# Performance work log

Hardware: AMD Instinct MI355X
Metric: run time of the kernel (lower is better)

The kernel has to match this reference:

```python
import jax, jax.numpy as jnp
import numpy as np

EMBED, HEADS, LEVELS, POINTS, FFN = 256, 8, 4, 4, 1024
HD = EMBED // HEADS


def layer_norm(x, g, b, eps=1e-5):
    m = jnp.mean(x, axis=-1, keepdims=True)
    v = jnp.mean((x - m) ** 2, axis=-1, keepdims=True)
    return (x - m) / jnp.sqrt(v + eps) * g + b


def ms_deform_attn_core(value, shapes_np, loc, attn):
    # value: (B, nk, H, hd); loc: (B, nq, H, L, P, 2) normalized [0,1]; attn: (B, nq, H, L, P)
    B, nq = loc.shape[0], loc.shape[1]
    splits = np.cumsum(shapes_np[:, 0] * shapes_np[:, 1])[:-1]
    vals = jnp.split(value, splits, axis=1)
    out = jnp.zeros((B, HEADS, nq, HD), value.dtype)
    for l in range(LEVELS):
        Hl, Wl = int(shapes_np[l, 0]), int(shapes_np[l, 1])
        v = vals[l].transpose(0, 2, 1, 3)                     # (B, H, Hl*Wl, hd)
        x = loc[:, :, :, l, :, 0] * Wl - 0.5                  # (B, nq, H, P) pixel coords
        y = loc[:, :, :, l, :, 1] * Hl - 0.5
        x0 = jnp.floor(x); y0 = jnp.floor(y)
        fx = x - x0; fy = y - y0
        x0i = x0.astype(jnp.int32); y0i = y0.astype(jnp.int32)
        acc = jnp.zeros((B, HEADS, nq * POINTS, HD), value.dtype)
        for dx, dy, w in ((0, 0, (1 - fx) * (1 - fy)), (1, 0, fx * (1 - fy)),
                          (0, 1, (1 - fx) * fy), (1, 1, fx * fy)):
            xi = x0i + dx; yi = y0i + dy
            valid = (xi >= 0) & (xi < Wl) & (yi >= 0) & (yi < Hl)
            idx = jnp.clip(yi, 0, Hl - 1) * Wl + jnp.clip(xi, 0, Wl - 1)  # (B, nq, H, P)
            idx_f = idx.transpose(0, 2, 1, 3).reshape(B, HEADS, -1)
            g = jnp.take_along_axis(v, idx_f[..., None], axis=2)          # (B, H, nq*P, hd)
            wv = jnp.where(valid, w, 0.0).transpose(0, 2, 1, 3).reshape(B, HEADS, -1, 1)
            acc = acc + g * wv
        aw = attn[:, :, :, l].transpose(0, 2, 1, 3).reshape(B, HEADS, -1, 1)
        out = out + (acc * aw).reshape(B, HEADS, nq, POINTS, HD).sum(3)
    return out.transpose(0, 2, 1, 3).reshape(B, nq, EMBED)


def setup_inputs() -> dict:
    key = jax.random.key(0)
    ks = jax.random.split(key, 20)
    B = 2
    shapes = np.array([[136, 136], [68, 68], [34, 34], [17, 17]], np.int32)
    nk = int((shapes[:, 0] * shapes[:, 1]).sum())  # 24565
    lsi = np.concatenate([[0], np.cumsum(shapes[:, 0] * shapes[:, 1])[:-1]]).astype(np.int32)

    def lin(k, i, o):
        return jax.random.normal(k, (i, o), jnp.float32) * 0.02

    return {
        "src": jax.random.normal(ks[0], (B, nk, EMBED), jnp.float32),
        "reference_points": jax.random.uniform(ks[1], (B, nk, LEVELS, 2), jnp.float32),
        "spatial_shapes": jnp.asarray(shapes),
        "level_start_index": jnp.asarray(lsi),
        "w_off": lin(ks[2], EMBED, HEADS * LEVELS * POINTS * 2),
        "b_off": jax.random.normal(ks[3], (HEADS * LEVELS * POINTS * 2,), jnp.float32) * 0.5,
        "w_att": lin(ks[4], EMBED, HEADS * LEVELS * POINTS),
        "b_att": jnp.zeros((HEADS * LEVELS * POINTS,), jnp.float32),
        "w_val": lin(ks[5], EMBED, EMBED), "b_val": jnp.zeros((EMBED,), jnp.float32),
        "w_out": lin(ks[6], EMBED, EMBED), "b_out": jnp.zeros((EMBED,), jnp.float32),
        "g1": jnp.ones((EMBED,), jnp.float32), "bt1": jnp.zeros((EMBED,), jnp.float32),
        "w1": lin(ks[7], EMBED, FFN), "b1": jnp.zeros((FFN,), jnp.float32),
        "w2": lin(ks[8], FFN, EMBED), "b2": jnp.zeros((EMBED,), jnp.float32),
        "g2": jnp.ones((EMBED,), jnp.float32), "bt2": jnp.zeros((EMBED,), jnp.float32),
    }


def reference(src, reference_points, spatial_shapes, level_start_index,
              w_off, b_off, w_att, b_att, w_val, b_val, w_out, b_out,
              g1, bt1, w1, b1, w2, b2, g2, bt2):
    B, nq, D = src.shape
    shapes_np = np.asarray(spatial_shapes)
    # projections
    value = (src @ w_val + b_val).reshape(B, nq, HEADS, HD)
    off = (src @ w_off + b_off).reshape(B, nq, HEADS, LEVELS, POINTS, 2)
    attn = (src @ w_att + b_att).reshape(B, nq, HEADS, LEVELS * POINTS)
    attn = jax.nn.softmax(attn, axis=-1).reshape(B, nq, HEADS, LEVELS, POINTS)
    # sampling locations: ref + offset / [W, H] per level
    normalizer = jnp.asarray(shapes_np[:, ::-1].copy(), src.dtype)  # (L, 2) = [W, H]
    loc = reference_points[:, :, None, :, None, :] + off / normalizer[None, None, None, :, None, :]
    attn_out = ms_deform_attn_core(value, shapes_np, loc, attn) @ w_out + b_out
    x = layer_norm(src + attn_out, g1, bt1)
    ffn = jax.nn.relu(x @ w1 + b1) @ w2 + b2
    return layer_norm(x + ffn, g2, bt2)
```

## Files before the change

### kernel.cpp

```cpp
#include <hip/hip_runtime.h>
#include <math.h>

#define EMBED 256
#define HEADS 8
#define LEVELS 4
#define POINTS 4
#define FFNDIM 1024

typedef float f32x4 __attribute__((ext_vector_type(4)));
typedef float f32x2 __attribute__((ext_vector_type(2)));
typedef __bf16 bf16x8 __attribute__((ext_vector_type(8)));

static __device__ __forceinline__ float4 ld4f(const float* p) {
    return *reinterpret_cast<const float4*>(p);
}
static __device__ __forceinline__ unsigned short f2bf(float f) {
    unsigned int u = __float_as_uint(f);
    unsigned int r = (u + 0x7fffu + ((u >> 16) & 1u)) >> 16;
    return (unsigned short)r;
}
static __device__ __forceinline__ float bf2f(unsigned short u) {
    return __uint_as_float((unsigned int)u << 16);
}
static __device__ __forceinline__ f32x2 pkfma(f32x2 a, f32x2 b, f32x2 c) {
#if __has_builtin(__builtin_elementwise_fma)
    return __builtin_elementwise_fma(a, b, c);
#else
    f32x2 r; r.x = fmaf(a.x, b.x, c.x); r.y = fmaf(a.y, b.y, c.y); return r;
#endif
}
static __device__ __forceinline__
void gl_lds16(const unsigned short* g, unsigned short* l) {
    __builtin_amdgcn_global_load_lds(
        (const __attribute__((address_space(1))) unsigned int*)g,
        (__attribute__((address_space(3))) unsigned int*)l, 16, 0, 0);
}

__global__ __launch_bounds__(256)
void k_cvt_src(const float* __restrict__ src, unsigned short* __restrict__ dst, int n)
{
    int i = (blockIdx.x * 256 + threadIdx.x) * 4;
    const int stride = gridDim.x * 1024;
    for (; i < n; i += stride) {
        float4 v = ld4f(src + i);
        ushort4 o;
        o.x = f2bf(v.x); o.y = f2bf(v.y); o.z = f2bf(v.z); o.w = f2bf(v.w);
        *reinterpret_cast<ushort4*>(dst + i) = o;
    }
}

__global__ __launch_bounds__(256)
void k_cvt_w(const float* __restrict__ wv, const float* __restrict__ wo,
             const float* __restrict__ wa, const float* __restrict__ wout,
             const float* __restrict__ w1, const float* __restrict__ w2,
             unsigned short* __restrict__ wcat, unsigned short* __restrict__ woutt,
             unsigned short* __restrict__ w1t, unsigned short* __restrict__ w2t)
{
    const int total = 163840 + 65536 + 262144 + 262144;
    for (int gid = blockIdx.x * 256 + threadIdx.x; gid < total; gid += gridDim.x * 256) {
        int local = gid;
        float f; unsigned short* dst;
        if (local < 163840) {
            int n = local >> 8, k = local & 255;
            if (n < 256)      f = wv[k * 256 + n];
            else if (n < 512) f = wo[k * 256 + (n - 256)];
            else              f = wa[k * 128 + (n - 512)];
            dst = wcat + local;
        } else if ((local -= 163840) < 65536) {
            int n = local >> 8, k = local & 255;
            f = wout[k * 256 + n];
            dst = woutt + local;
        } else if ((local -= 65536) < 262144) {
            int n = local >> 8, k = local & 255;
            f = w1[k * 1024 + n];
            dst = w1t + local;
        } else {
            local -= 262144;
            int n = local >> 10, k = local & 1023;
            f = w2[k * 256 + n];
            dst = w2t + local;
        }
        *dst = f2bf(f);
    }
}


#define GEMM_STAGE(Aptr, ASTR, Wptr, WSTR, kcexp)                              \
    {                                                                          \
        int row = (wid << 3) + (lane >> 3);                                    \
        int slot = (lane & 7) ^ (row & 7);                                     \
        gl_lds16(Aptr + (size_t)(m0 + row) * ASTR + (kcexp) * 64 + slot * 8,   \
                 a_s + (size_t)(wid << 3) * 64);                               \
    }                                                                          \
    _Pragma("unroll")                                                          \
    for (int rnd = 0; rnd < 4; ++rnd) {                                        \
        int row = (rnd << 6) + (wid << 3) + (lane >> 3);                       \
        int slot = (lane & 7) ^ (row & 7);                                     \
        gl_lds16(Wptr + (size_t)(n0 + row) * WSTR + (kcexp) * 64 + slot * 8,   \
                 w_s + (size_t)((rnd << 6) + (wid << 3)) * 64);                \
    }

#define GEMM_FRAGS_MFMA                                                        \
    {                                                                          \
        bf16x8 af[2][2], bfr[4][2];                                            \
        const int ksb = (lane >> 4);                                           \
        _Pragma("unroll")                                                      \
        for (int i = 0; i < 2; ++i) {                                          \
            int m = wm * 32 + i * 16 + cl;                                     \
            _Pragma("unroll")                                                  \
            for (int kk = 0; kk < 2; ++kk) {                                   \
                int phys = (kk * 4 + ksb) ^ (m & 7);                           \
                af[i][kk] = *reinterpret_cast<const bf16x8*>(                  \
                    a_s + m * 64 + phys * 8);                                  \
            }                                                                  \
        }                                                                      \
        _Pragma("unroll")                                                      \
        for (int j = 0; j < 4; ++j) {                                          \
            int n = wn * 64 + j * 16 + cl;                                     \
            _Pragma("unroll")                                                  \
            for (int kk = 0; kk < 2; ++kk) {                                   \
                int phys = (kk * 4 + ksb) ^ (n & 7);                           \
                bfr[j][kk] = *reinterpret_cast<const bf16x8*>(                 \
                    w_s + n * 64 + phys * 8);                                  \
            }                                                                  \
        }                                                                      \
        _Pragma("unroll")                                                      \
        for (int kk = 0; kk < 2; ++kk)                                         \
            _Pragma("unroll")                                                  \
            for (int i = 0; i < 2; ++i)                                        \
                _Pragma("unroll")                                              \
                for (int j = 0; j < 4; ++j)                                    \
                    acc[i][j] = __builtin_amdgcn_mfma_f32_16x16x32_bf16(       \
                        af[i][kk], bfr[j][kk], acc[i][j], 0, 0, 0);            \
    }

__global__ __launch_bounds__(512)
void k_proj(const unsigned short* __restrict__ A, const unsigned short* __restrict__ Wt,
            const float* __restrict__ b_val, const float* __restrict__ b_off,
            const float* __restrict__ b_att,
            unsigned short* __restrict__ value, unsigned short* __restrict__ offr,
            unsigned short* __restrict__ attw, int M, int nk)
{
    __shared__ __align__(16) unsigned short smem[20480];
    unsigned short* a_s = smem;
    unsigned short* w_s = smem + 4096;
    const int tid = threadIdx.x;
    const int m0 = blockIdx.x * 64;
    const int y = blockIdx.y;
    const int n0 = y * 256;
    const int lane = tid & 63, wid = tid >> 6;
    const int wm = wid >> 2, wn = wid & 3;
    const int cl = lane & 15, r4 = (lane >> 4) * 4;

    f32x4 acc[2][4] = {};

    for (int kc = 0; kc < 4; ++kc) {
        __syncthreads();
        GEMM_STAGE(A, 256, Wt, 256, kc)
        __syncthreads();
        GEMM_FRAGS_MFMA
    }

    if (y < 2) {
        const float* bias = (y == 0) ? b_val : b_off;
        __syncthreads();
        #pragma unroll
        for (int j = 0; j < 4; ++j) {
            int col = wn * 64 + j * 16 + cl;
            float bv = bias[col];
            #pragma unroll
            for (int i = 0; i < 2; ++i)
                #pragma unroll
                for (int r = 0; r < 4; ++r)
                    smem[(wm * 32 + i * 16 + r4 + r) * 264 + col] = f2bf(acc[i][j][r] + bv);
        }
        __syncthreads();
        if (y == 0) {
            #pragma unroll
            for (int t = 0; t < 4; ++t) {
                int idx = tid + t * 512;
                int row = idx >> 5, cu = idx & 31;
                int grow = m0 + row;
                if (grow < M) {
                    int b = grow >= nk;
                    int pix = grow - (b ? nk : 0);
                    int hh = cu >> 2, ch = (cu & 3) * 8;
                    *reinterpret_cast<uint4*>(
                        value + ((size_t)(b * 8 + hh) * nk + pix) * 32 + ch) =
                        *reinterpret_cast<const uint4*>(smem + row * 264 + cu * 8);
                }
            }
        } else {
            #pragma unroll
            for (int t = 0; t < 4; ++t) {
                int idx = tid + t * 512;
                int row = idx >> 5, cu = idx & 31;
                int grow = m0 + row;
                if (grow < M)
                    *reinterpret_cast<uint4*>(offr + (size_t)grow * 256 + cu * 8) =
                        *reinterpret_cast<const uint4*>(smem + row * 264 + cu * 8);
            }
        }
    } else {
        if (wn < 2) {
            #pragma unroll
            for (int j = 0; j < 4; ++j) {
                int a = wn * 64 + j * 16 + cl;
                float bv = b_att[a];
                #pragma unroll
                for (int i = 0; i < 2; ++i) {
                    #pragma unroll
                    for (int r = 0; r < 4; ++r) {
                        float v = acc[i][j][r] + bv;
                        float mx = v;
                        mx = fmaxf(mx, __shfl_xor(mx, 1));
                        mx = fmaxf(mx, __shfl_xor(mx, 2));
                        mx = fmaxf(mx, __shfl_xor(mx, 4));
                        mx = fmaxf(mx, __shfl_xor(mx, 8));
                        float e = __expf(v - mx);
                        float s = e;
                        s += __shfl_xor(s, 1);
                        s += __shfl_xor(s, 2);
                        s += __shfl_xor(s, 4);
                        s += __shfl_xor(s, 8);
                        acc[i][j][r] = e / s;
                    }
                }
            }
        }
        __syncthreads();
        if (wn < 2) {
            #pragma unroll
            for (int j = 0; j < 4; ++j) {
                int a = wn * 64 + j * 16 + cl;
                #pragma unroll
                for (int i = 0; i < 2; ++i)
                    #pragma unroll
                    for (int r = 0; r < 4; ++r)
                        smem[(wm * 32 + i * 16 + r4 + r) * 136 + a] = f2bf(acc[i][j][r]);
            }
        }
        __syncthreads();
        #pragma unroll
        for (int t = 0; t < 2; ++t) {
            int idx = tid + t * 512;
            int row = idx >> 4, cu = idx & 15;
            int grow = m0 + row;
            if (grow < M)
                *reinterpret_cast<uint4*>(attw + (size_t)grow * 128 + cu * 8) =
                    *reinterpret_cast<const uint4*>(smem + row * 136 + cu * 8);
        }
    }
}

__global__ __launch_bounds__(256)
void k_sample(const unsigned short* __restrict__ value,
              const unsigned short* __restrict__ offr,
              const unsigned short* __restrict__ attw,
              const float* __restrict__ ref,
              const int* __restrict__ shapes, const int* __restrict__ lsi,
              unsigned short* __restrict__ core, int M)
{
    __shared__ int2 iw_s[8][8][65];
    const int tid = threadIdx.x;
    const int tok0 = blockIdx.x * 8;
    const int nk = lsi[3] + shapes[6] * shapes[7];

    #pragma unroll
    for (int q = 0; q < 4; ++q) {
        const int task = tid + q * 256;
        const int tl = task >> 7;
        const int rest = task & 127;
        const int l = (rest >> 2) & 3;
        const int lp = rest & 15;
        const int hh = rest >> 4;
        const int tok = tok0 + tl;
        int2 out[4];
        if (tok < M) {
            const int Hl = shapes[l * 2], Wl = shapes[l * 2 + 1];
            const int bh = ((tok >= nk) ? 8 : 0) + hh;
            const int pbase = bh * nk + lsi[l];
            const float rx = ref[(size_t)tok * 8 + l * 2];
            const float ry = ref[(size_t)tok * 8 + l * 2 + 1];
            const unsigned int oxy =
                *reinterpret_cast<const unsigned int*>(offr + (size_t)tok * 256 + rest * 2);
            const float ox = bf2f((unsigned short)(oxy & 0xffffu));
            const float oy = bf2f((unsigned short)(oxy >> 16));
            const float aw = bf2f(attw[(size_t)tok * 128 + rest]);
            const float x = fmaf(rx, (float)Wl, ox) - 0.5f;
            const float y = fmaf(ry, (float)Hl, oy) - 0.5f;
            const float x0f = floorf(x), y0f = floorf(y);
            const float fx = x - x0f, fy = y - y0f;
            const int x0 = (int)x0f, y0 = (int)y0f;
            #pragma unroll
            for (int t = 0; t < 4; ++t) {
                const int dx = t & 1, dy = t >> 1;
                const int xi = x0 + dx, yi = y0 + dy;
                const bool valid = (xi >= 0) & (xi < Wl) & (yi >= 0) & (yi < Hl);
                const float w = (dx ? fx : 1.f - fx) * (dy ? fy : 1.f - fy) * aw;
                const int xc = min(max(xi, 0), Wl - 1);
                const int yc = min(max(yi, 0), Hl - 1);
                out[t].x = (pbase + yc * Wl + xc) * 16;
                out[t].y = __float_as_int(valid ? w : 0.f);
            }
        } else {
            #pragma unroll
            for (int t = 0; t < 4; ++t) out[t] = make_int2(0, 0);
        }
        #pragma unroll
        for (int t = 0; t < 4; ++t)
            iw_s[tl][hh][lp * 4 + t] = out[t];
    }
    __syncthreads();

    const int tl = tid >> 5;
    const int h = (tid >> 2) & 7;
    const int dp = tid & 3;
    const int tok = tok0 + tl;
    const unsigned int* vu = reinterpret_cast<const unsigned int*>(value) + dp * 4;
    const int2* pt = &iw_s[tl][h][0];
    f32x2 a0 = {0.f, 0.f}, a1 = {0.f, 0.f};
    f32x2 a2 = {0.f, 0.f}, a3 = {0.f, 0.f};
    #pragma unroll 16
    for (int q = 0; q < 64; ++q) {
        const int2 iw = pt[q];
        const float w = __int_as_float(iw.y);
        const f32x2 w2 = {w, w};
        const uint4 v = *reinterpret_cast<const uint4*>(vu + (size_t)(unsigned)iw.x);
        const f32x2 v0 = {__uint_as_float(v.x << 16), __uint_as_float(v.x & 0xffff0000u)};
        const f32x2 v1 = {__uint_as_float(v.y << 16), __uint_as_float(v.y & 0xffff0000u)};
        const f32x2 v2 = {__uint_as_float(v.z << 16), __uint_as_float(v.z & 0xffff0000u)};
        const f32x2 v3 = {__uint_as_float(v.w << 16), __uint_as_float(v.w & 0xffff0000u)};
        a0 = pkfma(v0, w2, a0);
        a1 = pkfma(v1, w2, a1);
        a2 = pkfma(v2, w2, a2);
        a3 = pkfma(v3, w2, a3);
    }
    if (tok < M) {
        uint4 o;
        o.x = (unsigned int)f2bf(a0.x) | ((unsigned int)f2bf(a0.y) << 16);
        o.y = (unsigned int)f2bf(a1.x) | ((unsigned int)f2bf(a1.y) << 16);
        o.z = (unsigned int)f2bf(a2.x) | ((unsigned int)f2bf(a2.y) << 16);
        o.w = (unsigned int)f2bf(a3.x) | ((unsigned int)f2bf(a3.y) << 16);
        *reinterpret_cast<uint4*>(core + (size_t)tok * 256 + h * 32 + dp * 8) = o;
    }
}

__global__ __launch_bounds__(512)
void k_oproj(const unsigned short* __restrict__ A, const unsigned short* __restrict__ Wt,
             const float* __restrict__ b_out, const float* __restrict__ src,
             const float* __restrict__ g1, const float* __restrict__ bt1,
             unsigned short* __restrict__ X, int M)
{
    __shared__ __align__(16) unsigned short smem[20480];
    unsigned short* a_s = smem;
    unsigned short* w_s = smem + 4096;
    __shared__ float red[64 * 8];
    __shared__ float mr[64 * 2];
    const int tid = threadIdx.x;
    const int m0 = blockIdx.x * 64;
    const int n0 = 0;
    const int lane = tid & 63, wid = tid >> 6;
    const int wm = wid >> 2, wn = wid & 3;
    const int cl = lane & 15, r4 = (lane >> 4) * 4;

    f32x4 acc[2][4] = {};

    for (int kc = 0; kc < 4; ++kc) {
        __syncthreads();
        GEMM_STAGE(A, 256, Wt, 256, kc)
        __syncthreads();
        GEMM_FRAGS_MFMA
    }

    #pragma unroll
    for (int j = 0; j < 4; ++j) {
        int col = wn * 64 + j * 16 + cl;
        float bv = b_out[col];
        #pragma unroll
        for (int i = 0; i < 2; ++i) {
            int mb = wm * 32 + i * 16 + r4;
            #pragma unroll
            for (int r = 0; r < 4; ++r) {
                int row = m0 + mb + r;
                float sv = (row < M) ? src[(size_t)row * 256 + col] : 0.f;
                acc[i][j][r] += bv + sv;
            }
        }
    }
    #pragma unroll
    for (int i = 0; i < 2; ++i)
        #pragma unroll
        for (int r = 0; r < 4; ++r) {
            float s1 = 0.f, s2 = 0.f;
            #pragma unroll
            for (int j = 0; j < 4; ++j) { float t = acc[i][j][r]; s1 += t; s2 += t * t; }
            s1 += __shfl_xor(s1, 1); s2 += __shfl_xor(s2, 1);
            s1 += __shfl_xor(s1, 2); s2 += __shfl_xor(s2, 2);
            s1 += __shfl_xor(s1, 4); s2 += __shfl_xor(s2, 4);
            s1 += __shfl_xor(s1, 8); s2 += __shfl_xor(s2, 8);
            if (cl == 0) {
                int rr = wm * 32 + i * 16 + r4 + r;
                red[(rr * 4 + wn) * 2 + 0] = s1;
                red[(rr * 4 + wn) * 2 + 1] = s2;
            }
        }
    __syncthreads();
    if (tid < 64) {
        float s1 = red[tid * 8] + red[tid * 8 + 2] + red[tid * 8 + 4] + red[tid * 8 + 6];
        float s2 = red[tid * 8 + 1] + red[tid * 8 + 3] + red[tid * 8 + 5] + red[tid * 8 + 7];
        float mu = s1 * (1.f / 256.f);
        mr[tid * 2] = mu;
        mr[tid * 2 + 1] = rsqrtf(fmaxf(s2 * (1.f / 256.f) - mu * mu, 0.f) + 1e-5f);
    }
    __syncthreads();
    #pragma unroll
    for (int j = 0; j < 4; ++j) {
        int col = wn * 64 + j * 16 + cl;
        float gv = g1[col], bt = bt1[col];
        #pragma unroll
        for (int i = 0; i < 2; ++i)
            #pragma unroll
            for (int r = 0; r < 4; ++r) {
                int rr = wm * 32 + i * 16 + r4 + r;
                smem[rr * 264 + col] =
                    f2bf((acc[i][j][r] - mr[rr * 2]) * mr[rr * 2 + 1] * gv + bt);
            }
    }
    __syncthreads();
    #pragma unroll
    for (int t = 0; t < 4; ++t) {
        int idx = tid + t * 512;
        int row = idx >> 5, cu = idx & 31;
        int grow = m0 + row;
        if (grow < M)
            *reinterpret_cast<uint4*>(X + (size_t)grow * 256 + cu * 8) =
                *reinterpret_cast<const uint4*>(smem + row * 264 + cu * 8);
    }
}

__global__ __launch_bounds__(512)
void k_ffn1(const unsigned short* __restrict__ A, const unsigned short* __restrict__ W1t,
            const float* __restrict__ B1, unsigned short* __restrict__ h, int M)
{
    __shared__ __align__(16) unsigned short smem[20480];
    unsigned short* a_s = smem;
    unsigned short* w_s = smem + 4096;
    const int tid = threadIdx.x;
    const int m0 = blockIdx.x * 64;
    const int n0 = blockIdx.y * 256;
    const int lane = tid & 63, wid = tid >> 6;
    const int wm = wid >> 2, wn = wid & 3;
    const int cl = lane & 15, r4 = (lane >> 4) * 4;

    f32x4 acc[2][4] = {};

    for (int kc = 0; kc < 4; ++kc) {
        __syncthreads();
        GEMM_STAGE(A, 256, W1t, 256, kc)
        __syncthreads();
        GEMM_FRAGS_MFMA
    }

    __syncthreads();
    #pragma unroll
    for (int j = 0; j < 4; ++j) {
        int col = wn * 64 + j * 16 + cl;
        float bv = B1[n0 + col];
        #pragma unroll
        for (int i = 0; i < 2; ++i)
            #pragma unroll
            for (int r = 0; r < 4; ++r)
                smem[(wm * 32 + i * 16 + r4 + r) * 264 + col] =
                    f2bf(fmaxf(acc[i][j][r] + bv, 0.f));
    }
    __syncthreads();
    #pragma unroll
    for (int t = 0; t < 4; ++t) {
        int idx = tid + t * 512;
        int row = idx >> 5, cu = idx & 31;
        int grow = m0 + row;
        if (grow < M)
            *reinterpret_cast<uint4*>(h + (size_t)grow * 1024 + n0 + cu * 8) =
                *reinterpret_cast<const uint4*>(smem + row * 264 + cu * 8);
    }
}

__global__ __launch_bounds__(512)
void k_ffn2(const unsigned short* __restrict__ h, const unsigned short* __restrict__ W2t,
            const float* __restrict__ B2, const unsigned short* __restrict__ Xbf,
            const float* __restrict__ G2, const float* __restrict__ BT2,
            float* __restrict__ OUT, int M)
{
    __shared__ __align__(16) unsigned short smem[20480];
    unsigned short* a_s = smem;
    unsigned short* w_s = smem + 4096;
    __shared__ float red[64 * 8];
    __shared__ float mr[64 * 2];
    const int tid = threadIdx.x;
    const int m0 = blockIdx.x * 64;
    const int n0 = 0;
    const int lane = tid & 63, wid = tid >> 6;
    const int wm = wid >> 2, wn = wid & 3;
    const int cl = lane & 15, r4 = (lane >> 4) * 4;

    f32x4 acc[2][4] = {};

    for (int kc = 0; kc < 16; ++kc) {
        __syncthreads();
        GEMM_STAGE(h, 1024, W2t, 1024, kc)
        __syncthreads();
        GEMM_FRAGS_MFMA
    }

    #pragma unroll
    for (int j = 0; j < 4; ++j) {
        int col = wn * 64 + j * 16 + cl;
        float bv = B2[col];
        #pragma unroll
        for (int i = 0; i < 2; ++i) {
            int mb = wm * 32 + i * 16 + r4;
            #pragma unroll
            for (int r = 0; r < 4; ++r) {
                int row = m0 + mb + r;
                float xv = (row < M) ? bf2f(Xbf[(size_t)row * 256 + col]) : 0.f;
                acc[i][j][r] += bv + xv;
            }
        }
    }
    #pragma unroll
    for (int i = 0; i < 2; ++i)
        #pragma unroll
        for (int r = 0; r < 4; ++r) {
            float s1 = 0.f, s2 = 0.f;
            #pragma unroll
            for (int j = 0; j < 4; ++j) { float t = acc[i][j][r]; s1 += t; s2 += t * t; }
            s1 += __shfl_xor(s1, 1); s2 += __shfl_xor(s2, 1);
            s1 += __shfl_xor(s1, 2); s2 += __shfl_xor(s2, 2);
            s1 += __shfl_xor(s1, 4); s2 += __shfl_xor(s2, 4);
            s1 += __shfl_xor(s1, 8); s2 += __shfl_xor(s2, 8);
            if (cl == 0) {
                int rr = wm * 32 + i * 16 + r4 + r;
                red[(rr * 4 + wn) * 2 + 0] = s1;
                red[(rr * 4 + wn) * 2 + 1] = s2;
            }
        }
    __syncthreads();
    if (tid < 64) {
        float s1 = red[tid * 8] + red[tid * 8 + 2] + red[tid * 8 + 4] + red[tid * 8 + 6];
        float s2 = red[tid * 8 + 1] + red[tid * 8 + 3] + red[tid * 8 + 5] + red[tid * 8 + 7];
        float mu = s1 * (1.f / 256.f);
        mr[tid * 2] = mu;
        mr[tid * 2 + 1] = rsqrtf(fmaxf(s2 * (1.f / 256.f) - mu * mu, 0.f) + 1e-5f);
    }
    __syncthreads();
    #pragma unroll
    for (int j = 0; j < 4; ++j) {
        int col = wn * 64 + j * 16 + cl;
        float gv = G2[col], bt = BT2[col];
        #pragma unroll
        for (int i = 0; i < 2; ++i) {
            int mb = wm * 32 + i * 16 + r4;
            #pragma unroll
            for (int r = 0; r < 4; ++r) {
                int rr = mb + r, row = m0 + rr;
                if (row < M)
                    OUT[(size_t)row * 256 + col] =
                        (acc[i][j][r] - mr[rr * 2]) * mr[rr * 2 + 1] * gv + bt;
            }
        }
    }
}

extern "C" void kernel_launch(void* const* d_in, const int* in_sizes, int n_in,
                              void* d_out, int out_size, void* d_ws, size_t ws_size,
                              hipStream_t stream) {
    const float* src    = (const float*)d_in[0];
    const float* ref    = (const float*)d_in[1];
    const int*   shapes = (const int*)d_in[2];
    const int*   lsi    = (const int*)d_in[3];
    const float* b_off  = (const float*)d_in[5];
    const float* b_att  = (const float*)d_in[7];
    const float* b_val  = (const float*)d_in[9];
    const float* b_out  = (const float*)d_in[11];
    const float* g1     = (const float*)d_in[12];
    const float* bt1    = (const float*)d_in[13];
    const float* b1     = (const float*)d_in[15];
    const float* b2     = (const float*)d_in[17];
    const float* g2     = (const float*)d_in[18];
    const float* bt2    = (const float*)d_in[19];
    const float* w_off  = (const float*)d_in[4];
    const float* w_att  = (const float*)d_in[6];
    const float* w_val  = (const float*)d_in[8];
    const float* w_out  = (const float*)d_in[10];
    const float* w1     = (const float*)d_in[14];
    const float* w2     = (const float*)d_in[16];

    const int M = in_sizes[0] / EMBED;
    const int nk = M / 2;
    const size_t M256 = (size_t)M * 256;

    unsigned short* w16     = (unsigned short*)d_ws;
    unsigned short* src_bf  = w16;
    unsigned short* value_bf = src_bf + M256;
    unsigned short* offr_bf = value_bf + M256;
    unsigned short* core_bf = offr_bf + M256;
    unsigned short* x_bf    = core_bf + M256;
    unsigned short* attw_bf = x_bf + M256;
    unsigned short* wcat    = attw_bf + (size_t)M * 128;
    unsigned short* woutt   = wcat + 163840;
    unsigned short* w1t     = woutt + 65536;
    unsigned short* w2t     = w1t + 262144;
    unsigned short* h_bf    = w16;

    const int gb64 = (M + 63) / 64;
    const int gbS = (M + 7) / 8;

    k_cvt_src<<<4096, 256, 0, stream>>>(src, src_bf, M * 256);
    k_cvt_w<<<2944, 256, 0, stream>>>(w_val, w_off, w_att, w_out, w1, w2,
                                      wcat, woutt, w1t, w2t);
    k_proj<<<dim3(gb64, 3), 512, 0, stream>>>(src_bf, wcat, b_val, b_off, b_att,
                                              value_bf, offr_bf, attw_bf, M, nk);
    k_sample<<<gbS, 256, 0, stream>>>(value_bf, offr_bf, attw_bf, ref, shapes, lsi,
                                      core_bf, M);
    k_oproj<<<gb64, 512, 0, stream>>>(core_bf, woutt, b_out, src, g1, bt1, x_bf, M);
    k_ffn1<<<dim3(gb64, 4), 512, 0, stream>>>(x_bf, w1t, b1, h_bf, M);
    k_ffn2<<<gb64, 512, 0, stream>>>(h_bf, w2t, b2, x_bf, g2, bt2,
                                     (float*)d_out, M);
}
```

Measured before the change: 280.0 us.

## Remap deformable sampling blocks to one batch-head over 64 consecutive queries

Measured after the change: 258.8 us. -7.6%, faster.

```diff
diff --git a/kernel.cpp b/kernel.cpp
--- a/kernel.cpp
+++ b/kernel.cpp
@@ -261,32 +261,32 @@
               const int* __restrict__ shapes, const int* __restrict__ lsi,
               unsigned short* __restrict__ core, int M)
 {
-    __shared__ int2 iw_s[8][8][65];
+    __shared__ int2 iw_s[64][65];
     const int tid = threadIdx.x;
-    const int tok0 = blockIdx.x * 8;
+    const int bh = blockIdx.x & 15;
+    const int grp = blockIdx.x >> 4;
+    const int b = bh >> 3, h = bh & 7;
     const int nk = lsi[3] + shapes[6] * shapes[7];
-
-    #pragma unroll
-    for (int q = 0; q < 4; ++q) {
-        const int task = tid + q * 256;
-        const int tl = task >> 7;
-        const int rest = task & 127;
-        const int l = (rest >> 2) & 3;
-        const int lp = rest & 15;
-        const int hh = rest >> 4;
-        const int tok = tok0 + tl;
+    const int tok0 = grp * 64;
+
+    #pragma unroll
+    for (int rnd = 0; rnd < 4; ++rnd) {
+        const int lp = tid & 15;
+        const int tk = rnd * 16 + (tid >> 4);
+        const int l = lp >> 2;
+        const int pix0 = tok0 + tk;
         int2 out[4];
-        if (tok < M) {
+        if (pix0 < nk) {
+            const int token = b * nk + pix0;
             const int Hl = shapes[l * 2], Wl = shapes[l * 2 + 1];
-            const int bh = ((tok >= nk) ? 8 : 0) + hh;
             const int pbase = bh * nk + lsi[l];
-            const float rx = ref[(size_t)tok * 8 + l * 2];
-            const float ry = ref[(size_t)tok * 8 + l * 2 + 1];
-            const unsigned int oxy =
-                *reinterpret_cast<const unsigned int*>(offr + (size_t)tok * 256 + rest * 2);
+            const float rx = ref[(size_t)token * 8 + l * 2];
+            const float ry = ref[(size_t)token * 8 + l * 2 + 1];
+            const unsigned int oxy = *reinterpret_cast<const unsigned int*>(
+                offr + (size_t)token * 256 + (h * 16 + lp) * 2);
             const float ox = bf2f((unsigned short)(oxy & 0xffffu));
             const float oy = bf2f((unsigned short)(oxy >> 16));
-            const float aw = bf2f(attw[(size_t)tok * 128 + rest]);
+            const float aw = bf2f(attw[(size_t)token * 128 + h * 16 + lp]);
             const float x = fmaf(rx, (float)Wl, ox) - 0.5f;
             const float y = fmaf(ry, (float)Hl, oy) - 0.5f;
             const float x0f = floorf(x), y0f = floorf(y);
@@ -309,21 +309,19 @@
         }
         #pragma unroll
         for (int t = 0; t < 4; ++t)
-            iw_s[tl][hh][lp * 4 + t] = out[t];
-    }
-    __syncthreads();
-
-    const int tl = tid >> 5;
-    const int h = (tid >> 2) & 7;
+            iw_s[lp * 4 + t][tk] = out[t];
+    }
+    __syncthreads();
+
+    const int tk = tid >> 2;
     const int dp = tid & 3;
-    const int tok = tok0 + tl;
+    const int pix = tok0 + tk;
     const unsigned int* vu = reinterpret_cast<const unsigned int*>(value) + dp * 4;
-    const int2* pt = &iw_s[tl][h][0];
     f32x2 a0 = {0.f, 0.f}, a1 = {0.f, 0.f};
     f32x2 a2 = {0.f, 0.f}, a3 = {0.f, 0.f};
     #pragma unroll 16
     for (int q = 0; q < 64; ++q) {
-        const int2 iw = pt[q];
+        const int2 iw = iw_s[q][tk];
         const float w = __int_as_float(iw.y);
         const f32x2 w2 = {w, w};
         const uint4 v = *reinterpret_cast<const uint4*>(vu + (size_t)(unsigned)iw.x);
@@ -336,13 +334,14 @@
         a2 = pkfma(v2, w2, a2);
         a3 = pkfma(v3, w2, a3);
     }
-    if (tok < M) {
+    if (pix < nk) {
         uint4 o;
         o.x = (unsigned int)f2bf(a0.x) | ((unsigned int)f2bf(a0.y) << 16);
         o.y = (unsigned int)f2bf(a1.x) | ((unsigned int)f2bf(a1.y) << 16);
         o.z = (unsigned int)f2bf(a2.x) | ((unsigned int)f2bf(a2.y) << 16);
         o.w = (unsigned int)f2bf(a3.x) | ((unsigned int)f2bf(a3.y) << 16);
-        *reinterpret_cast<uint4*>(core + (size_t)tok * 256 + h * 32 + dp * 8) = o;
+        *reinterpret_cast<uint4*>(
+            core + (size_t)(b * nk + pix) * 256 + h * 32 + dp * 8) = o;
     }
 }
 
@@ -614,15 +613,15 @@
     unsigned short* h_bf    = w16;
 
     const int gb64 = (M + 63) / 64;
-    const int gbS = (M + 7) / 8;
+    const int ngrp = (nk + 63) / 64;
 
     k_cvt_src<<<4096, 256, 0, stream>>>(src, src_bf, M * 256);
     k_cvt_w<<<2944, 256, 0, stream>>>(w_val, w_off, w_att, w_out, w1, w2,
                                       wcat, woutt, w1t, w2t);
     k_proj<<<dim3(gb64, 3), 512, 0, stream>>>(src_bf, wcat, b_val, b_off, b_att,
                                               value_bf, offr_bf, attw_bf, M, nk);
-    k_sample<<<gbS, 256, 0, stream>>>(value_bf, offr_bf, attw_bf, ref, shapes, lsi,
-                                      core_bf, M);
+    k_sample<<<ngrp * 16, 256, 0, stream>>>(value_bf, offr_bf, attw_bf, ref,
+                                            shapes, lsi, core_bf, M);
     k_oproj<<<gb64, 512, 0, stream>>>(core_bf, woutt, b_out, src, g1, bt1, x_bf, M);
     k_ffn1<<<dim3(gb64, 4), 512, 0, stream>>>(x_bf, w1t, b1, h_bf, M);
     k_ffn2<<<gb64, 512, 0, stream>>>(h_bf, w2t, b2, x_bf, g2, bt2,
```
